# Kernel optimization log

Measured on AMD Instinct MI355X. Metric: run time of the kernel, lower is better.

Reference implementation:

```python
import jax, jax.numpy as jnp
import numpy as np

DN = ('NCHW', 'OIHW', 'NCHW')

def _conv(x, w, b, pad):
    y = jax.lax.conv_general_dilated(x, w, (1, 1), pad, dimension_numbers=DN)
    return y + b[None, :, None, None]

def setup_inputs() -> dict:
    key = jax.random.key(0)
    ks = jax.random.split(key, 8)
    B, C, H, W = 8, 256, 64, 64
    C8 = C // 8
    return {
        'x': jax.random.normal(ks[0], (B, C, H, W), jnp.float32),
        'wq': jax.random.normal(ks[1], (C8, C, 1, 3), jnp.float32) * 0.02,
        'bq': jax.random.normal(ks[2], (C8,), jnp.float32) * 0.02,
        'wk': jax.random.normal(ks[3], (C8, C, 3, 1), jnp.float32) * 0.02,
        'bk': jax.random.normal(ks[4], (C8,), jnp.float32) * 0.02,
        'wv': jax.random.normal(ks[5], (C, C, 1, 1), jnp.float32) * 0.02,
        'bv': jax.random.normal(ks[6], (C,), jnp.float32) * 0.02,
        'gamma': jax.random.normal(ks[7], (1,), jnp.float32),
    }

def reference(x, wq, bq, wk, bk, wv, bv, gamma):
    B, C, H, W = x.shape
    N = H * W
    # q: (1,3) kernel, pad (0,1); k: (3,1) kernel, pad (1,0); v: 1x1
    q = _conv(x, wq, bq, [(0, 0), (1, 1)]).reshape(B, -1, N)  # B, C/8, N
    k = _conv(x, wk, bk, [(1, 1), (0, 0)]).reshape(B, -1, N)  # B, C/8, N
    v = _conv(x, wv, bv, [(0, 0), (0, 0)]).reshape(B, C, N)   # B, C, N
    affinity = jnp.einsum('bci,bcj->bij', q, k)               # B, N, N
    affinity = jax.nn.softmax(affinity, axis=-1)
    # weights = v @ affinity^T  ->  (B, C, N)
    weights = jnp.einsum('bcj,bij->bci', v, affinity).reshape(B, C, H, W)
    return gamma[0] * weights + x
```

## Files before the change

### kernel.cpp

```cpp
#include <hip/hip_runtime.h>
#include <math.h>

#define BB 8
#define CCH 256
#define C8 32
#define NN 4096
#define LOG2E 1.44269504f

typedef unsigned short us;
typedef __attribute__((ext_vector_type(8))) short bf16x8;
typedef __attribute__((ext_vector_type(4))) float f32x4;
typedef __attribute__((ext_vector_type(16))) float f32x16;

static __device__ __forceinline__ us f2bf(float f) {
  union { float f; unsigned u; } v; v.f = f;
  unsigned r = v.u + 0x7fffu + ((v.u >> 16) & 1u);
  return (us)(r >> 16);
}
static __device__ __forceinline__ us f2bf_rhu(float f) {
  return (us)((__float_as_uint(f) + 0x8000u) >> 16);
}
template <int CTRL>
static __device__ __forceinline__ float dpp_mv(float x) {
  return __int_as_float(
      __builtin_amdgcn_update_dpp(0, __float_as_int(x), CTRL, 0xF, 0xF, false));
}
static __device__ __forceinline__ float rowsum16(float t) {
  t += dpp_mv<0x121>(t);
  t += dpp_mv<0x122>(t);
  t += dpp_mv<0x124>(t);
  t += dpp_mv<0x128>(t);
  return t;
}

__global__ __launch_bounds__(256) void prep_kernel(
    const float* __restrict__ x, const float* __restrict__ wq,
    const float* __restrict__ wk, const float* __restrict__ wv,
    us* __restrict__ xT, us* __restrict__ wqc, us* __restrict__ wkc,
    us* __restrict__ wvb) {
  __shared__ __align__(16) us lt[64 * 68];
  int bid = blockIdx.x;
  int tid = threadIdx.x;
  if (bid < 2048) {
    int b = bid >> 8, cb = (bid >> 6) & 3, nb = bid & 63;
    const float* xb = x + (((size_t)(b * 256 + cb * 64)) << 12);
    int nl = tid & 63, ch = tid >> 6;
#pragma unroll
    for (int p = 0; p < 16; p++) {
      int c = p * 4 + ch;
      lt[nl * 68 + c] = f2bf(xb[((size_t)c << 12) + (nb * 64 + nl)]);
    }
    __syncthreads();
    us* xTb = xT + (((size_t)b << 12) + nb * 64) * 256 + cb * 64;
    int cw = tid & 7, nr0 = tid >> 3;
#pragma unroll
    for (int p2 = 0; p2 < 2; p2++) {
      int nr = p2 * 32 + nr0;
      uint2 lo = *(const uint2*)&lt[nr * 68 + cw * 8];
      uint2 hi = *(const uint2*)&lt[nr * 68 + cw * 8 + 4];
      *(uint4*)&xTb[(size_t)nr * 256 + cw * 8] = make_uint4(lo.x, lo.y, hi.x, hi.y);
    }
  } else {
    int idx = (bid - 2048) * 256 + tid;
    if (idx < 24576) {
      int oc = idx / 768, r = idx % 768, t = r >> 8, ic = r & 255;
      wqc[idx] = f2bf(wq[(oc * 256 + ic) * 3 + t] * LOG2E);
    } else if (idx < 49152) {
      int j = idx - 24576;
      int oc = j / 768, r = j % 768, t = r >> 8, ic = r & 255;
      wkc[j] = f2bf(wk[(oc * 256 + ic) * 3 + t]);
    } else if (idx < 114688) {
      int j = idx - 49152;
      wvb[j] = f2bf(wv[j]);
    }
  }
}

__global__ __launch_bounds__(256) void conv_kernel(
    const us* __restrict__ xT, const us* __restrict__ wqc,
    const us* __restrict__ wkc, const float* __restrict__ bq,
    const float* __restrict__ bk, const us* __restrict__ wvb,
    const float* __restrict__ bv, us* __restrict__ qT, us* __restrict__ kT,
    us* __restrict__ vblk) {
  int tid = threadIdx.x, lane = tid & 63, w = tid >> 6;
  int l15 = lane & 15, quad = lane >> 4;
  if (blockIdx.x < 512) {
    int bid = blockIdx.x;
    int b = bid & 7, rt = bid >> 3;
    int n0 = rt * 64, y = rt;
    bool isq = (w < 2);
    int m0 = (w & 1) * 16;
    const us* wc = isq ? wqc : wkc;
    const us* xTb = xT + (((size_t)b << 12) * 256);
    f32x4 acc[4];
#pragma unroll
    for (int nt = 0; nt < 4; nt++) acc[nt] = (f32x4){0.f, 0.f, 0.f, 0.f};
#pragma unroll
    for (int t = 0; t < 3; t++) {
      bool killT = (!isq) && ((t == 0 && y == 0) || (t == 2 && y == 63));
      if (!killT) {
        int dn = isq ? (t - 1) : (t - 1) * 64;
#pragma unroll
        for (int k8 = 0; k8 < 8; k8++) {
          int kloc = t * 256 + k8 * 32 + quad * 8;
          bf16x8 af = *(const bf16x8*)(wc + (size_t)(m0 + l15) * 768 + kloc);
          int ic = k8 * 32 + quad * 8;
#pragma unroll
          for (int nt = 0; nt < 4; nt++) {
            int nl = nt * 16 + l15;
            int ns = n0 + nl + dn;
            ns = ns < 0 ? 0 : (ns > 4095 ? 4095 : ns);
            bf16x8 bf = *(const bf16x8*)(xTb + (size_t)ns * 256 + ic);
            if (isq && ((t == 0 && nl == 0) || (t == 2 && nl == 63)))
              bf = (bf16x8){0, 0, 0, 0, 0, 0, 0, 0};
            acc[nt] = __builtin_amdgcn_mfma_f32_16x16x32_bf16(af, bf, acc[nt], 0, 0, 0);
          }
        }
      }
    }
    const float* bias = isq ? bq : bk;
    float bsc = isq ? LOG2E : 1.0f;
    us* outp = (isq ? qT : kT) + (((size_t)b << 12) * 32);
    float b0 = bias[m0 + quad * 4 + 0] * bsc;
    float b1 = bias[m0 + quad * 4 + 1] * bsc;
    float b2 = bias[m0 + quad * 4 + 2] * bsc;
    float b3 = bias[m0 + quad * 4 + 3] * bsc;
#pragma unroll
    for (int nt = 0; nt < 4; nt++) {
      int n = n0 + nt * 16 + l15;
      unsigned lo = (unsigned)f2bf(acc[nt][0] + b0) | ((unsigned)f2bf(acc[nt][1] + b1) << 16);
      unsigned hi = (unsigned)f2bf(acc[nt][2] + b2) | ((unsigned)f2bf(acc[nt][3] + b3) << 16);
      *(uint2*)(outp + (size_t)n * 32 + m0 + quad * 4) = make_uint2(lo, hi);
    }
  } else {
    int bid = blockIdx.x - 512;
    int b = bid & 7, nt0 = bid >> 3;
    int n0 = nt0 * 64;
    const us* xTb = xT + (((size_t)b << 12) * 256);
    f32x4 acc[4][4];
#pragma unroll
    for (int ct = 0; ct < 4; ct++)
#pragma unroll
      for (int nt = 0; nt < 4; nt++) acc[ct][nt] = (f32x4){0.f, 0.f, 0.f, 0.f};
#pragma unroll
    for (int kk = 0; kk < 8; kk++) {
      bf16x8 bfr[4];
#pragma unroll
      for (int nt = 0; nt < 4; nt++)
        bfr[nt] = *(const bf16x8*)(xTb + (size_t)(n0 + nt * 16 + l15) * 256 + kk * 32 + quad * 8);
#pragma unroll
      for (int ct = 0; ct < 4; ct++) {
        bf16x8 af = *(const bf16x8*)(wvb + (size_t)(w * 64 + ct * 16 + l15) * 256 + kk * 32 + quad * 8);
#pragma unroll
        for (int nt = 0; nt < 4; nt++)
          acc[ct][nt] = __builtin_amdgcn_mfma_f32_16x16x32_bf16(af, bfr[nt], acc[ct][nt], 0, 0, 0);
      }
    }
    us* vb = vblk + ((size_t)b << 20);
#pragma unroll
    for (int ct = 0; ct < 4; ct++) {
#pragma unroll
      for (int r = 0; r < 4; r++) {
        int oc = w * 64 + ct * 16 + quad * 4 + r;
        float bvv = bv[oc];
#pragma unroll
        for (int nt = 0; nt < 4; nt++) {
          vb[((size_t)((n0 >> 4) + nt) * 256 + oc) * 16 + l15] = f2bf(acc[ct][nt][r] + bvv);
        }
      }
    }
  }
}

__global__ __launch_bounds__(512, 4) void attn_kernel(
    const float* __restrict__ x, const us* __restrict__ qT,
    const us* __restrict__ kT, const us* __restrict__ vblk,
    const float* __restrict__ gamma_p, float* __restrict__ out) {
  __shared__ __align__(16) us pb[2][64 * 72];
  __shared__ float lpart[2][64];

  int tid = threadIdx.x, lane = tid & 63, w = tid >> 6;
  int l15 = lane & 15, quad = lane >> 4;
  int l31 = lane & 31, h32 = lane >> 5;
  int tw = w & 3, jh = w >> 2;

  int bid = blockIdx.x;
  int b = bid & 7, i0 = (bid >> 3) * 64;

  const us* qTb = qT + (((size_t)b << 12) * 32);
  const us* kTb = kT + (((size_t)b << 12) * 32);
  const us* vbb = vblk + ((size_t)b << 20);

  bf16x8 qf = *(const bf16x8*)(qTb + (size_t)(i0 + tw * 16 + l15) * 32 + quad * 8);

  float lr[4] = {0.f, 0.f, 0.f, 0.f};
  f32x16 o[2];
#pragma unroll
  for (int it = 0; it < 2; it++)
#pragma unroll
    for (int rg = 0; rg < 16; rg++) o[it][rg] = 0.f;

  int bu = 0;
  for (int jt = 0; jt < 64; jt++) {
    int j0 = jt * 64;
    bf16x8 kf0 = *(const bf16x8*)(kTb + (size_t)(j0 + jh * 32 + l15) * 32 + quad * 8);
    bf16x8 kf1 = *(const bf16x8*)(kTb + (size_t)(j0 + jh * 32 + 16 + l15) * 32 + quad * 8);
    bf16x8 vf[4];
#pragma unroll
    for (int ks = 0; ks < 4; ks++)
      vf[ks] = *(const bf16x8*)(vbb + ((size_t)((j0 >> 4) + ks) * 256 + w * 32 + l31) * 16 + h32 * 8);
    f32x4 s0 = __builtin_amdgcn_mfma_f32_16x16x32_bf16(qf, kf0, (f32x4){0.f, 0.f, 0.f, 0.f}, 0, 0, 0);
    f32x4 s1 = __builtin_amdgcn_mfma_f32_16x16x32_bf16(qf, kf1, (f32x4){0.f, 0.f, 0.f, 0.f}, 0, 0, 0);
    us* pw = &pb[bu][(tw * 16 + quad * 4) * 72 + jh * 32 + l15];
#pragma unroll
    for (int r = 0; r < 4; r++) {
      float p0 = __builtin_amdgcn_exp2f(s0[r]);
      float p1 = __builtin_amdgcn_exp2f(s1[r]);
      lr[r] += p0 + p1;
      pw[r * 72] = f2bf_rhu(p0);
      pw[r * 72 + 16] = f2bf_rhu(p1);
    }
    __syncthreads();
#pragma unroll
    for (int ks = 0; ks < 4; ks++) {
      bf16x8 pf0 = *(const bf16x8*)&pb[bu][(size_t)l31 * 72 + ks * 16 + h32 * 8];
      bf16x8 pf1 = *(const bf16x8*)&pb[bu][(size_t)(32 + l31) * 72 + ks * 16 + h32 * 8];
      o[0] = __builtin_amdgcn_mfma_f32_32x32x16_bf16(vf[ks], pf0, o[0], 0, 0, 0);
      o[1] = __builtin_amdgcn_mfma_f32_32x32x16_bf16(vf[ks], pf1, o[1], 0, 0, 0);
    }
    bu ^= 1;
  }

  float ls[4];
#pragma unroll
  for (int r = 0; r < 4; r++) ls[r] = rowsum16(lr[r]);
  if (l15 == 0) {
#pragma unroll
    for (int r = 0; r < 4; r++) lpart[jh][tw * 16 + quad * 4 + r] = ls[r];
  }
  __syncthreads();
  float g = gamma_p[0];
  const float* xb = x + ((size_t)b << 20);
  float* ob = out + ((size_t)b << 20);
  float gl[2];
#pragma unroll
  for (int it = 0; it < 2; it++) {
    int i = it * 32 + l31;
    gl[it] = g / (lpart[0][i] + lpart[1][i]);
  }
#pragma unroll
  for (int it = 0; it < 2; it++) {
    int i = i0 + it * 32 + l31;
#pragma unroll
    for (int rg = 0; rg < 16; rg++) {
      int c = w * 32 + ((rg & 3) + 8 * (rg >> 2) + 4 * h32);
      size_t idx = ((size_t)c << 12) + i;
      ob[idx] = o[it][rg] * gl[it] + xb[idx];
    }
  }
}

extern "C" void kernel_launch(void* const* d_in, const int* in_sizes, int n_in,
                              void* d_out, int out_size, void* d_ws, size_t ws_size,
                              hipStream_t stream) {
  const float* x = (const float*)d_in[0];
  const float* wq = (const float*)d_in[1];
  const float* bq = (const float*)d_in[2];
  const float* wk = (const float*)d_in[3];
  const float* bk = (const float*)d_in[4];
  const float* wv = (const float*)d_in[5];
  const float* bv = (const float*)d_in[6];
  const float* gamma = (const float*)d_in[7];
  float* out = (float*)d_out;

  us* xT = (us*)d_ws;
  us* qT = xT + (size_t)8388608;
  us* kT = qT + (size_t)1048576;
  us* vblk = kT + (size_t)1048576;
  us* wqc = vblk + (size_t)8388608;
  us* wkc = wqc + (size_t)24576;
  us* wvb = wkc + (size_t)24576;

  prep_kernel<<<2496, 256, 0, stream>>>(x, wq, wk, wv, xT, wqc, wkc, wvb);
  conv_kernel<<<1024, 256, 0, stream>>>(xT, wqc, wkc, bq, bk, wvb, bv, qT, kT, vblk);
  attn_kernel<<<512, 512, 0, stream>>>(x, qT, kT, vblk, gamma, out);
}
```

Before: 235.4 us.

## Widen attention key tile to 128 and vectorize V projection stores

The attention loop now processes 128 keys per iteration instead of 64, halving the number of block barriers and doubling the MFMA work and loads per synchronization. The P staging buffer in shared memory grows to match, which cuts occupancy headroom and raises register pressure from extra K/V fragments. In the V-projection kernel the MFMA operands are swapped so each lane holds four consecutive positions, letting the bf16 results be packed and written as one 8-byte store instead of four scalar stores.

```diff
diff --git a/kernel.cpp b/kernel.cpp
--- a/kernel.cpp
+++ b/kernel.cpp
@@ -150,23 +150,22 @@
         bfr[nt] = *(const bf16x8*)(xTb + (size_t)(n0 + nt * 16 + l15) * 256 + kk * 32 + quad * 8);
 #pragma unroll
       for (int ct = 0; ct < 4; ct++) {
-        bf16x8 af = *(const bf16x8*)(wvb + (size_t)(w * 64 + ct * 16 + l15) * 256 + kk * 32 + quad * 8);
+        bf16x8 wf = *(const bf16x8*)(wvb + (size_t)(w * 64 + ct * 16 + l15) * 256 + kk * 32 + quad * 8);
 #pragma unroll
         for (int nt = 0; nt < 4; nt++)
-          acc[ct][nt] = __builtin_amdgcn_mfma_f32_16x16x32_bf16(af, bfr[nt], acc[ct][nt], 0, 0, 0);
+          acc[ct][nt] = __builtin_amdgcn_mfma_f32_16x16x32_bf16(bfr[nt], wf, acc[ct][nt], 0, 0, 0);
       }
     }
     us* vb = vblk + ((size_t)b << 20);
 #pragma unroll
     for (int ct = 0; ct < 4; ct++) {
-#pragma unroll
-      for (int r = 0; r < 4; r++) {
-        int oc = w * 64 + ct * 16 + quad * 4 + r;
-        float bvv = bv[oc];
-#pragma unroll
-        for (int nt = 0; nt < 4; nt++) {
-          vb[((size_t)((n0 >> 4) + nt) * 256 + oc) * 16 + l15] = f2bf(acc[ct][nt][r] + bvv);
-        }
+      int oc = w * 64 + ct * 16 + l15;
+      float bvv = bv[oc];
+#pragma unroll
+      for (int nt = 0; nt < 4; nt++) {
+        unsigned lo = (unsigned)f2bf(acc[ct][nt][0] + bvv) | ((unsigned)f2bf(acc[ct][nt][1] + bvv) << 16);
+        unsigned hi = (unsigned)f2bf(acc[ct][nt][2] + bvv) | ((unsigned)f2bf(acc[ct][nt][3] + bvv) << 16);
+        *(uint2*)(vb + ((size_t)((n0 >> 4) + nt) * 256 + oc) * 16 + quad * 4) = make_uint2(lo, hi);
       }
     }
   }
@@ -176,7 +175,7 @@
     const float* __restrict__ x, const us* __restrict__ qT,
     const us* __restrict__ kT, const us* __restrict__ vblk,
     const float* __restrict__ gamma_p, float* __restrict__ out) {
-  __shared__ __align__(16) us pb[2][64 * 72];
+  __shared__ __align__(16) us pb[2][64 * 136];
   __shared__ float lpart[2][64];
 
   int tid = threadIdx.x, lane = tid & 63, w = tid >> 6;
@@ -201,30 +200,34 @@
     for (int rg = 0; rg < 16; rg++) o[it][rg] = 0.f;
 
   int bu = 0;
-  for (int jt = 0; jt < 64; jt++) {
-    int j0 = jt * 64;
-    bf16x8 kf0 = *(const bf16x8*)(kTb + (size_t)(j0 + jh * 32 + l15) * 32 + quad * 8);
-    bf16x8 kf1 = *(const bf16x8*)(kTb + (size_t)(j0 + jh * 32 + 16 + l15) * 32 + quad * 8);
-    bf16x8 vf[4];
-#pragma unroll
-    for (int ks = 0; ks < 4; ks++)
+  for (int jt = 0; jt < 32; jt++) {
+    int j0 = jt * 128;
+    bf16x8 kf[4];
+#pragma unroll
+    for (int j2 = 0; j2 < 4; j2++)
+      kf[j2] = *(const bf16x8*)(kTb + (size_t)(j0 + jh * 64 + j2 * 16 + l15) * 32 + quad * 8);
+    bf16x8 vf[8];
+#pragma unroll
+    for (int ks = 0; ks < 8; ks++)
       vf[ks] = *(const bf16x8*)(vbb + ((size_t)((j0 >> 4) + ks) * 256 + w * 32 + l31) * 16 + h32 * 8);
-    f32x4 s0 = __builtin_amdgcn_mfma_f32_16x16x32_bf16(qf, kf0, (f32x4){0.f, 0.f, 0.f, 0.f}, 0, 0, 0);
-    f32x4 s1 = __builtin_amdgcn_mfma_f32_16x16x32_bf16(qf, kf1, (f32x4){0.f, 0.f, 0.f, 0.f}, 0, 0, 0);
-    us* pw = &pb[bu][(tw * 16 + quad * 4) * 72 + jh * 32 + l15];
-#pragma unroll
-    for (int r = 0; r < 4; r++) {
-      float p0 = __builtin_amdgcn_exp2f(s0[r]);
-      float p1 = __builtin_amdgcn_exp2f(s1[r]);
-      lr[r] += p0 + p1;
-      pw[r * 72] = f2bf_rhu(p0);
-      pw[r * 72 + 16] = f2bf_rhu(p1);
-    }
+    f32x4 s[4];
+#pragma unroll
+    for (int j2 = 0; j2 < 4; j2++)
+      s[j2] = __builtin_amdgcn_mfma_f32_16x16x32_bf16(qf, kf[j2], (f32x4){0.f, 0.f, 0.f, 0.f}, 0, 0, 0);
+    us* pw = &pb[bu][(tw * 16 + quad * 4) * 136 + jh * 64 + l15];
+#pragma unroll
+    for (int j2 = 0; j2 < 4; j2++)
+#pragma unroll
+      for (int r = 0; r < 4; r++) {
+        float p = __builtin_amdgcn_exp2f(s[j2][r]);
+        lr[r] += p;
+        pw[r * 136 + j2 * 16] = f2bf_rhu(p);
+      }
     __syncthreads();
 #pragma unroll
-    for (int ks = 0; ks < 4; ks++) {
-      bf16x8 pf0 = *(const bf16x8*)&pb[bu][(size_t)l31 * 72 + ks * 16 + h32 * 8];
-      bf16x8 pf1 = *(const bf16x8*)&pb[bu][(size_t)(32 + l31) * 72 + ks * 16 + h32 * 8];
+    for (int ks = 0; ks < 8; ks++) {
+      bf16x8 pf0 = *(const bf16x8*)&pb[bu][(size_t)l31 * 136 + ks * 16 + h32 * 8];
+      bf16x8 pf1 = *(const bf16x8*)&pb[bu][(size_t)(32 + l31) * 136 + ks * 16 + h32 * 8];
       o[0] = __builtin_amdgcn_mfma_f32_32x32x16_bf16(vf[ks], pf0, o[0], 0, 0, 0);
       o[1] = __builtin_amdgcn_mfma_f32_32x32x16_bf16(vf[ks], pf1, o[1], 0, 0, 0);
     }
```

Result: no change. 236.7 us (+0.6%).
